# Kernel optimization log

Hardware: AMD Instinct MI355X
Metric: run time of the kernel (lower is better)

## Reference

```python
import jax, jax.numpy as jnp
import numpy as np
from jax import lax

T, B = 128, 256          # rollout length x num envs
H, W, C = 7, 7, 3        # minigrid obs
HID = 128                # lstm hidden
NA = 7                   # actions
NFLAT = 64 * 4 * 4       # conv flatten (7->6->5->4)


def setup_inputs() -> dict:
    key = jax.random.key(0)
    ks = jax.random.split(key, 20)
    N = T * B
    obs = jax.random.randint(ks[0], (N, H, W, C), 0, 11).astype(jnp.float32)
    done = (jax.random.uniform(ks[1], (N,)) < 0.05).astype(jnp.float32)
    h0 = jnp.zeros((1, B, HID), jnp.float32)
    c0 = jnp.zeros((1, B, HID), jnp.float32)
    s = 0.1
    conv1_w = jax.random.normal(ks[2], (16, C, 2, 2)) * s
    conv1_b = jnp.zeros((16,), jnp.float32)
    conv2_w = jax.random.normal(ks[3], (32, 16, 2, 2)) * s
    conv2_b = jnp.zeros((32,), jnp.float32)
    conv3_w = jax.random.normal(ks[4], (64, 32, 2, 2)) * s
    conv3_b = jnp.zeros((64,), jnp.float32)
    w_ih = jax.random.normal(ks[5], (4 * HID, NFLAT)) * 0.03
    w_hh = jax.random.normal(ks[6], (4 * HID, HID)) * 0.08
    b_ih = jnp.zeros((4 * HID,), jnp.float32)
    b_hh = jnp.zeros((4 * HID,), jnp.float32)
    actor_w = jax.random.normal(ks[7], (NA, HID)) * 0.01
    actor_b = jnp.zeros((NA,), jnp.float32)
    critic_w = jax.random.normal(ks[8], (1, HID)) * 0.08
    critic_b = jnp.zeros((1,), jnp.float32)
    return dict(obs=obs, done=done, h0=h0, c0=c0,
                conv1_w=conv1_w, conv1_b=conv1_b,
                conv2_w=conv2_w, conv2_b=conv2_b,
                conv3_w=conv3_w, conv3_b=conv3_b,
                w_ih=w_ih, w_hh=w_hh, b_ih=b_ih, b_hh=b_hh,
                actor_w=actor_w, actor_b=actor_b,
                critic_w=critic_w, critic_b=critic_b)


def _conv(x, w, b):
    # x: [N, Cin, h, w], w: [Cout, Cin, 2, 2], VALID, stride 1
    y = lax.conv_general_dilated(x, w, (1, 1), 'VALID',
                                 dimension_numbers=('NCHW', 'OIHW', 'NCHW'))
    return jax.nn.relu(y + b[None, :, None, None])


def reference(obs, done, h0, c0,
              conv1_w, conv1_b, conv2_w, conv2_b, conv3_w, conv3_b,
              w_ih, w_hh, b_ih, b_hh, actor_w, actor_b, critic_w, critic_b):
    N = obs.shape[0]
    x = jnp.transpose(obs, (0, 3, 1, 2))            # NHWC -> NCHW
    x = _conv(x, conv1_w, conv1_b)
    x = _conv(x, conv2_w, conv2_b)
    x = _conv(x, conv3_w, conv3_b)
    feat = x.reshape(N, -1)                          # [T*B, 1024]

    nb = h0.shape[1]
    xs = feat.reshape(-1, nb, feat.shape[-1])        # [T, B, 1024]
    ds = done.reshape(-1, nb)                        # [T, B]
    bias = b_ih + b_hh

    def step(carry, inp):
        h, c = carry                                  # [B, HID]
        x_t, d_t = inp
        m = (1.0 - d_t)[:, None]
        h = m * h
        c = m * c
        gates = x_t @ w_ih.T + h @ w_hh.T + bias      # [B, 4*HID]
        i, f, g, o = jnp.split(gates, 4, axis=-1)     # torch gate order i,f,g,o
        i = jax.nn.sigmoid(i)
        f = jax.nn.sigmoid(f)
        g = jnp.tanh(g)
        o = jax.nn.sigmoid(o)
        c = f * c + i * g
        h = o * jnp.tanh(c)
        return (h, c), h

    (hT, cT), hs = lax.scan(step, (h0[0], c0[0]), (xs, ds))
    hid = hs.reshape(N, -1)                           # [T*B, HID]
    logits = hid @ actor_w.T + actor_b                # [T*B, NA]
    value = hid @ critic_w.T + critic_b               # [T*B, 1]
    out = jnp.concatenate([logits, value], axis=-1)   # [T*B, NA+1]
    return out, hT[None], cT[None]
```

## Files before the change

### kernel.cpp

```cpp
#include <hip/hip_runtime.h>
#include <hip/hip_bf16.h>


#define N_IMG   32768
#define T_LEN   128
#define B_ENV   256
#define HID     128

typedef _Float16 f16x8 __attribute__((ext_vector_type(8)));
typedef _Float16 f16x2 __attribute__((ext_vector_type(2)));
typedef float    f32x4 __attribute__((ext_vector_type(4)));
typedef unsigned short ushort8v __attribute__((ext_vector_type(8)));
typedef unsigned short ushort4v __attribute__((ext_vector_type(4)));

__device__ __forceinline__ float sigm_(float x) { return 1.0f / (1.0f + __expf(-x)); }
__device__ __forceinline__ float tanh_(float x) { return 2.0f / (1.0f + __expf(-2.0f * x)) - 1.0f; }

__device__ __forceinline__ unsigned short f2h(float x) {
    _Float16 h = (_Float16)x;
    union { _Float16 h; unsigned short u; } un; un.h = h;
    return un.u;
}

#if defined(__has_builtin)
#if __has_builtin(__builtin_amdgcn_fdot2)
#define HAVE_FDOT2 1
#endif
#endif

__device__ __forceinline__ float dot2_(f16x2 a, f16x2 b, float c) {
#ifdef HAVE_FDOT2
    return __builtin_amdgcn_fdot2(a, b, c, false);
#else
    c = fmaf((float)a[0], (float)b[0], c);
    return fmaf((float)a[1], (float)b[1], c);
#endif
}

#define P0(v) __builtin_shufflevector(v, v, 0, 1)
#define P1(v) __builtin_shufflevector(v, v, 2, 3)
#define P2(v) __builtin_shufflevector(v, v, 4, 5)
#define P3(v) __builtin_shufflevector(v, v, 6, 7)

__device__ __forceinline__ float bfly_sum4(float x) {
    int y = __builtin_amdgcn_update_dpp(0, __float_as_int(x), 0xB1, 0xF, 0xF, true);
    x += __int_as_float(y);
    y = __builtin_amdgcn_update_dpp(0, __float_as_int(x), 0x4E, 0xF, 0xF, true);
    return x + __int_as_float(y);
}

#define GLDS16(g, l) __builtin_amdgcn_global_load_lds( \
    (const __attribute__((address_space(1))) unsigned int*)(g), \
    (__attribute__((address_space(3))) unsigned int*)(l), 16, 0, 0)

__global__ void prep_wih(const float* __restrict__ w, unsigned short* __restrict__ wb)
{
    const int idx = blockIdx.x * 256 + threadIdx.x;
    const int np = idx >> 10, kk = idx & 1023;
    const int p = kk >> 6, co = kk & 63;
    const int g = np & 3, ci = np >> 2;
    const int n = g * 128 + ci;
    wb[idx] = f2h(w[n * 1024 + co * 16 + p]);
}

__global__ void prep_convw(const float* __restrict__ w2, const float* __restrict__ w3,
                           unsigned short* __restrict__ wb2g, unsigned short* __restrict__ wb3g)
{
    const int t = blockIdx.x * 256 + threadIdx.x;
    if (t < 2048) {
        const int j = t & 7, lane = (t >> 3) & 63, f = t >> 9;
        const int ky = f >> 1, ct = f & 1;
        const int k = ((lane >> 4) << 3) + j, kx = k >> 4, ci = k & 15;
        wb2g[t] = f2h(w2[(ct * 16 + (lane & 15)) * 64 + ci * 4 + ky * 2 + kx]);
    } else if (t < 10240) {
        const int u = t - 2048;
        const int j = u & 7, lane = (u >> 3) & 63, f = u >> 9;
        const int ct = f >> 2, pos = f & 3;
        const int ci = ((lane >> 4) << 3) + j;
        wb3g[u] = f2h(w3[(ct * 16 + (lane & 15)) * 128 + ci * 4 + pos]);
    }
}

__global__ void prep_whhr(const float* __restrict__ w_hh, unsigned short* __restrict__ whhr)
{
    const int idx = blockIdx.x * 256 + threadIdx.x;
    const int thr = idx >> 7, r = idx & 127;
    const int g = r >> 5, k = r & 31;
    const int ci = thr >> 2, s = thr & 3;
    whhr[idx] = f2h(w_hh[(g * 128 + ci) * 128 + s * 32 + k]);
}

__global__ __launch_bounds__(256, 2) void conv_fused(
    const float* __restrict__ obs,
    const float* __restrict__ w1, const float* __restrict__ b1,
    const float* __restrict__ b2, const float* __restrict__ b3,
    const unsigned short* __restrict__ wb2g,
    const unsigned short* __restrict__ wb3g,
    unsigned short* __restrict__ featb)
{
    __shared__ __align__(16) unsigned char u1[25856];
    __shared__ __align__(16) unsigned char u2[33024];
    __shared__ float w1s[192];
    __shared__ float b1s[16];

    float* s_obs = (float*)u1;
    unsigned short* c2s = (unsigned short*)u1;
    unsigned short* c1s = (unsigned short*)u2;
    unsigned short* c3s = (unsigned short*)u2;

    const int tid = threadIdx.x, lane = tid & 63, wv = tid >> 6;
    const int base = blockIdx.x * 16;

    if (tid < 192) w1s[tid] = w1[tid];
    if (tid < 16)  b1s[tid] = b1[tid];
    for (int i = tid; i < 16 * 147; i += 256) {
        const int im = i / 147, r = i - im * 147;
        s_obs[im * 148 + r] = obs[(size_t)(base + im) * 147 + r];
    }
    __syncthreads();

    {
        const int img = tid & 15;
        const float* ob = &s_obs[img * 148];
        for (int p = tid >> 4; p < 36; p += 16) {
            const int py = p / 6, px = p % 6;
            float o[12];
#pragma unroll
            for (int ky = 0; ky < 2; ky++)
#pragma unroll
                for (int kx = 0; kx < 2; kx++)
#pragma unroll
                    for (int cc = 0; cc < 3; cc++)
                        o[cc * 4 + ky * 2 + kx] = ob[((py + ky) * 7 + px + kx) * 3 + cc];
            unsigned short res[16];
#pragma unroll
            for (int ci = 0; ci < 16; ci++) {
                float a = b1s[ci];
#pragma unroll
                for (int q = 0; q < 12; q++) a = fmaf(o[q], w1s[ci * 12 + q], a);
                res[ci] = f2h(fmaxf(a, 0.0f));
            }
            *(ushort8v*)&c1s[img * 584 + p * 16]     = *(ushort8v*)&res[0];
            *(ushort8v*)&c1s[img * 584 + p * 16 + 8] = *(ushort8v*)&res[8];
        }
    }
    __syncthreads();

    {
        const int ct = wv & 1, par = wv >> 1;
        const int img = lane & 15, kq = lane >> 4;
        f16x8 wA[2];
        wA[0] = *(const f16x8*)&wb2g[(0 + ct) * 512 + lane * 8];
        wA[1] = *(const f16x8*)&wb2g[(2 + ct) * 512 + lane * 8];
        const float4 b2v = *(const float4*)&b2[ct * 16 + kq * 4];
#pragma unroll 2
        for (int p = par; p < 25; p += 2) {
            const int py = p / 5, px = p % 5;
            f32x4 acc = {0.f, 0.f, 0.f, 0.f};
#pragma unroll
            for (int ky = 0; ky < 2; ky++) {
                const int pix = (py + ky) * 6 + px + (kq >> 1);
                const f16x8 bv = *(const f16x8*)&c1s[img * 584 + pix * 16 + (kq & 1) * 8];
                acc = __builtin_amdgcn_mfma_f32_16x16x32_f16(wA[ky], bv, acc, 0, 0, 0);
            }
            unsigned short r4[4];
            r4[0] = f2h(fmaxf(acc[0] + b2v.x, 0.0f));
            r4[1] = f2h(fmaxf(acc[1] + b2v.y, 0.0f));
            r4[2] = f2h(fmaxf(acc[2] + b2v.z, 0.0f));
            r4[3] = f2h(fmaxf(acc[3] + b2v.w, 0.0f));
            *(ushort4v*)&c2s[img * 808 + p * 32 + ct * 16 + kq * 4] = *(ushort4v*)&r4[0];
        }
    }
    __syncthreads();

    {
        const int ct = wv;
        const int img = lane & 15, kq = lane >> 4;
        f16x8 wA3[4];
#pragma unroll
        for (int pos = 0; pos < 4; pos++)
            wA3[pos] = *(const f16x8*)&wb3g[(ct * 4 + pos) * 512 + lane * 8];
        const float4 b3v = *(const float4*)&b3[ct * 16 + kq * 4];
#pragma unroll 4
        for (int p = 0; p < 16; p++) {
            const int py = p >> 2, px = p & 3;
            f32x4 acc = {0.f, 0.f, 0.f, 0.f};
#pragma unroll
            for (int pos = 0; pos < 4; pos++) {
                const int pix = (py + (pos >> 1)) * 5 + px + (pos & 1);
                const f16x8 bv = *(const f16x8*)&c2s[img * 808 + pix * 32 + kq * 8];
                acc = __builtin_amdgcn_mfma_f32_16x16x32_f16(wA3[pos], bv, acc, 0, 0, 0);
            }
            unsigned short r4[4];
            r4[0] = f2h(fmaxf(acc[0] + b3v.x, 0.0f));
            r4[1] = f2h(fmaxf(acc[1] + b3v.y, 0.0f));
            r4[2] = f2h(fmaxf(acc[2] + b3v.z, 0.0f));
            r4[3] = f2h(fmaxf(acc[3] + b3v.w, 0.0f));
            *(ushort4v*)&c3s[img * 1032 + p * 64 + ct * 16 + kq * 4] = *(ushort4v*)&r4[0];
        }
    }
    __syncthreads();

#pragma unroll
    for (int i = 0; i < 8; i++) {
        const int gi = i * 2048 + tid * 8;
        const int img = gi >> 10, flat = gi & 1023;
        *(ushort8v*)&featb[(size_t)(base + img) * 1024 + flat] =
            *(const ushort8v*)&c3s[img * 1032 + flat];
    }
}

__global__ __launch_bounds__(256, 2) void gemm_xproj_mfma(
    const unsigned short* __restrict__ A,
    const unsigned short* __restrict__ W,
    float* __restrict__ C)
{
    __shared__ unsigned short As[128 * 32];
    __shared__ unsigned short Bs[128 * 32];

    const int tid  = threadIdx.x;
    const int bx = blockIdx.x & 3;
    const int by = blockIdx.x >> 2;
    const int m0 = by * 128, n0 = bx * 128;
    const int lane = tid & 63, wave = tid >> 6;
    const int wm = (wave >> 1) * 64, wn = (wave & 1) * 64;
    const int srow = tid >> 2, sseg = tid & 3;

    const unsigned short* Ag = A + (size_t)(m0 + srow) * 1024 + sseg * 8;
    const unsigned short* Wg = W + (size_t)(n0 + srow) * 1024 + sseg * 8;

    f32x4 acc[4][4];
#pragma unroll
    for (int i = 0; i < 4; i++)
#pragma unroll
        for (int j = 0; j < 4; j++) acc[i][j] = (f32x4){0.f, 0.f, 0.f, 0.f};

    const int fr = lane & 15, fq = lane >> 4;

    for (int k0 = 0; k0 < 1024; k0 += 32) {
        __syncthreads();
        GLDS16(Ag + k0,             (char*)As + tid * 16);
        GLDS16(Ag + k0 + 64 * 1024, (char*)As + tid * 16 + 4096);
        GLDS16(Wg + k0,             (char*)Bs + tid * 16);
        GLDS16(Wg + k0 + 64 * 1024, (char*)Bs + tid * 16 + 4096);
        __syncthreads();

        f16x8 af[4], bfv[4];
#pragma unroll
        for (int i = 0; i < 4; i++)
            af[i] = *(const f16x8*)&As[(wm + i * 16 + fr) * 32 + fq * 8];
#pragma unroll
        for (int j = 0; j < 4; j++)
            bfv[j] = *(const f16x8*)&Bs[(wn + j * 16 + fr) * 32 + fq * 8];
#pragma unroll
        for (int i = 0; i < 4; i++)
#pragma unroll
            for (int j = 0; j < 4; j++)
                acc[i][j] = __builtin_amdgcn_mfma_f32_16x16x32_f16(af[i], bfv[j], acc[i][j], 0, 0, 0);
    }

    const int cr = fq * 4, cc = fr;
#pragma unroll
    for (int i = 0; i < 4; i++) {
#pragma unroll
        for (int j = 0; j < 4; j++) {
            float* cp = &C[(size_t)(m0 + wm + i * 16 + cr) * 512 + (n0 + wn + j * 16 + cc)];
#pragma unroll
            for (int r = 0; r < 4; r++)
                cp[(size_t)r * 512] = acc[i][j][r];
        }
    }
}

__global__ __launch_bounds__(512) __attribute__((amdgpu_waves_per_eu(2, 2)))
void lstm_bfly(
    const float* __restrict__ xproj, const float* __restrict__ done,
    const float* __restrict__ h0, const float* __restrict__ c0,
    const unsigned short* __restrict__ whhr,
    const float* __restrict__ b_ih, const float* __restrict__ b_hh,
    float* __restrict__ hid, float* __restrict__ out)
{
    const int b   = blockIdx.x;
    const int tid = threadIdx.x;
    const int ci  = tid >> 2;
    const int s   = tid & 3;

    __shared__ __align__(16) _Float16 hbuf[2][HID];

    f16x8 w[4][4];
    {
        const unsigned short* wp = whhr + (size_t)tid * 128;
#pragma unroll
        for (int g = 0; g < 4; g++)
#pragma unroll
            for (int i = 0; i < 4; i++)
                w[g][i] = *(const f16x8*)&wp[g * 32 + i * 8];
    }
    const float bias_l = b_ih[s * 128 + ci] + b_hh[s * 128 + ci];

    float c = c0[b * HID + ci];
    float h = h0[b * HID + ci];
    float dcur = done[b];

    if (tid < HID)
        hbuf[0][tid] = (_Float16)(h0[b * HID + tid] * (1.0f - dcur));

    float xq = bias_l + xproj[(size_t)b * 512 + ci * 4 + s];
    __syncthreads();

#define DOTBLK(i, c0_, c1_, c2_, c3_)                                           \
    {                                                                           \
        const f16x8 hv8 = *(const f16x8*)&hbuf[p][s * 32 + (i) * 8];            \
        const f16x2 hp0 = P0(hv8), hp1 = P1(hv8), hp2 = P2(hv8), hp3 = P3(hv8); \
        c0_ = dot2_(P0(w[0][i]), hp0, c0_); c0_ = dot2_(P1(w[0][i]), hp1, c0_); \
        c0_ = dot2_(P2(w[0][i]), hp2, c0_); c0_ = dot2_(P3(w[0][i]), hp3, c0_); \
        c1_ = dot2_(P0(w[1][i]), hp0, c1_); c1_ = dot2_(P1(w[1][i]), hp1, c1_); \
        c1_ = dot2_(P2(w[1][i]), hp2, c1_); c1_ = dot2_(P3(w[1][i]), hp3, c1_); \
        c2_ = dot2_(P0(w[2][i]), hp0, c2_); c2_ = dot2_(P1(w[2][i]), hp1, c2_); \
        c2_ = dot2_(P2(w[2][i]), hp2, c2_); c2_ = dot2_(P3(w[2][i]), hp3, c2_); \
        c3_ = dot2_(P0(w[3][i]), hp0, c3_); c3_ = dot2_(P1(w[3][i]), hp1, c3_); \
        c3_ = dot2_(P2(w[3][i]), hp2, c3_); c3_ = dot2_(P3(w[3][i]), hp3, c3_); \
    }

    int p = 0;
    for (int t = 0; t < T_LEN; t++) {
        const int tn = (t + 1 < T_LEN) ? t + 1 : t;
        const float xqn = bias_l + xproj[((size_t)tn * B_ENV + b) * 512 + ci * 4 + s];
        const float dnn = done[tn * B_ENV + b];

        float a0 = (s == 0) ? xq : 0.0f;
        float a1 = (s == 1) ? xq : 0.0f;
        float a2 = (s == 2) ? xq : 0.0f;
        float a3 = (s == 3) ? xq : 0.0f;
        float b0 = 0.f, b1 = 0.f, b2 = 0.f, b3 = 0.f;
        DOTBLK(0, a0, a1, a2, a3)
        DOTBLK(1, b0, b1, b2, b3)
        DOTBLK(2, a0, a1, a2, a3)
        DOTBLK(3, b0, b1, b2, b3)
        a0 += b0; a1 += b1; a2 += b2; a3 += b3;

        a0 = bfly_sum4(a0); a1 = bfly_sum4(a1);
        a2 = bfly_sum4(a2); a3 = bfly_sum4(a3);

        const float gi = sigm_(a0), gf = sigm_(a1);
        const float gg = tanh_(a2), go = sigm_(a3);
        const float m = 1.0f - dcur;
        c = fmaf(gf, c * m, gi * gg);
        h = go * tanh_(c);

        if (s == 0) {
            hid[((size_t)t * B_ENV + b) * HID + ci] = h;
            hbuf[p ^ 1][ci] = (_Float16)(h * (1.0f - dnn));
        }

        xq = xqn; dcur = dnn; p ^= 1;
        __syncthreads();
    }

    if (s == 0) {
        out[262144 + b * HID + ci] = h;
        out[294912 + b * HID + ci] = c;
    }
#undef DOTBLK
}

__global__ __launch_bounds__(256, 2) void heads_kernel(
    const float* __restrict__ hid,
    const float* __restrict__ aw, const float* __restrict__ ab,
    const float* __restrict__ cw, const float* __restrict__ cb,
    float* __restrict__ out)
{
    __shared__ float hs[32 * 129];
    __shared__ float ws[8 * 130];
    __shared__ float bs[8];

    const int tid = threadIdx.x;
    const int n0 = blockIdx.x * 32;

    for (int i = tid; i < 1024; i += 256) {
        const int r = i >> 7, k = i & 127;
        ws[r * 130 + k] = (r < 7) ? aw[r * 128 + k] : cw[k];
    }
    if (tid < 8) bs[tid] = (tid < 7) ? ab[tid] : cb[0];
    for (int i = tid; i < 4096; i += 256) {
        const int r = i >> 7, k = i & 127;
        hs[r * 129 + k] = hid[(size_t)(n0 + r) * 128 + k];
    }
    __syncthreads();

    const int r = tid >> 3, jj = tid & 7;
    float acc = bs[jj];
    const float* hp = &hs[r * 129];
    const float* wp = &ws[jj * 130];
#pragma unroll
    for (int k = 0; k < 128; k++) acc = fmaf(hp[k], wp[k], acc);
    out[(size_t)(n0 + r) * 8 + jj] = acc;
}

extern "C" void kernel_launch(void* const* d_in, const int* in_sizes, int n_in,
                              void* d_out, int out_size, void* d_ws, size_t ws_size,
                              hipStream_t stream)
{
    (void)in_sizes; (void)n_in; (void)out_size; (void)ws_size;

    const float* obs  = (const float*)d_in[0];
    const float* done = (const float*)d_in[1];
    const float* h0   = (const float*)d_in[2];
    const float* c0   = (const float*)d_in[3];
    const float* w1   = (const float*)d_in[4];
    const float* b1   = (const float*)d_in[5];
    const float* w2   = (const float*)d_in[6];
    const float* b2   = (const float*)d_in[7];
    const float* w3   = (const float*)d_in[8];
    const float* b3   = (const float*)d_in[9];
    const float* w_ih = (const float*)d_in[10];
    const float* w_hh = (const float*)d_in[11];
    const float* b_ih = (const float*)d_in[12];
    const float* b_hh = (const float*)d_in[13];
    const float* aw   = (const float*)d_in[14];
    const float* ab   = (const float*)d_in[15];
    const float* cw   = (const float*)d_in[16];
    const float* cb   = (const float*)d_in[17];
    float* out = (float*)d_out;

    unsigned short* featb = (unsigned short*)d_ws;
    unsigned short* wb    = featb + 33554432ull;
    unsigned short* wb2g  = wb    + 524288ull;
    unsigned short* wb3g  = wb2g  + 2048ull;
    float* xproj = (float*)(wb3g + 8192ull + 2048ull);
    float* hid   = xproj + 16777216ull;
    unsigned short* whhr = (unsigned short*)(hid + 4194304ull);

    prep_wih<<<2048, 256, 0, stream>>>(w_ih, wb);
    prep_convw<<<40, 256, 0, stream>>>(w2, w3, wb2g, wb3g);
    prep_whhr<<<256, 256, 0, stream>>>(w_hh, whhr);
    conv_fused<<<2048, 256, 0, stream>>>(obs, w1, b1, b2, b3, wb2g, wb3g, featb);
    gemm_xproj_mfma<<<1024, 256, 0, stream>>>(featb, wb, xproj);
    lstm_bfly<<<256, 512, 0, stream>>>(xproj, done, h0, c0, whhr, b_ih, b_hh, hid, out);
    heads_kernel<<<1024, 256, 0, stream>>>(hid, aw, ab, cw, cb, out);
}
```

Baseline: 309.5 us.

## Double-buffer xproj GEMM, fuse prep kernels, fp16 hidden states, faster activations

Several independent changes. The sigmoid and tanh helpers now use the exp2 and reciprocal hardware builtins. The three weight-prep kernels are merged into one launch. The input-projection GEMM double-buffers its LDS tiles so the next K-slice loads while MFMAs run. The LSTM hidden-state history is stored as fp16 and widened back to fp32 in the heads kernel, halving that traffic at some precision cost. The LSTM's serial recurrence probably dominates total time, so the gains elsewhere may be small.

After: 281.6 us. -9.0%, faster.

```diff
diff --git a/kernel.cpp b/kernel.cpp
--- a/kernel.cpp
+++ b/kernel.cpp
@@ -13,8 +13,27 @@
 typedef unsigned short ushort8v __attribute__((ext_vector_type(8)));
 typedef unsigned short ushort4v __attribute__((ext_vector_type(4)));
 
-__device__ __forceinline__ float sigm_(float x) { return 1.0f / (1.0f + __expf(-x)); }
-__device__ __forceinline__ float tanh_(float x) { return 2.0f / (1.0f + __expf(-2.0f * x)) - 1.0f; }
+#if defined(__has_builtin)
+#if __has_builtin(__builtin_amdgcn_exp2f)
+#define FEXP2(x) __builtin_amdgcn_exp2f(x)
+#endif
+#if __has_builtin(__builtin_amdgcn_rcpf)
+#define FRCP(x) __builtin_amdgcn_rcpf(x)
+#endif
+#endif
+#ifndef FEXP2
+#define FEXP2(x) exp2f(x)
+#endif
+#ifndef FRCP
+#define FRCP(x) (1.0f / (x))
+#endif
+
+__device__ __forceinline__ float sigm_(float x) {
+    return FRCP(1.0f + FEXP2(-1.44269504f * x));
+}
+__device__ __forceinline__ float tanh_(float x) {
+    return fmaf(-2.0f, FRCP(1.0f + FEXP2(2.88539008f * x)), 1.0f);
+}
 
 __device__ __forceinline__ unsigned short f2h(float x) {
     _Float16 h = (_Float16)x;
@@ -53,41 +72,39 @@
     (const __attribute__((address_space(1))) unsigned int*)(g), \
     (__attribute__((address_space(3))) unsigned int*)(l), 16, 0, 0)
 
-__global__ void prep_wih(const float* __restrict__ w, unsigned short* __restrict__ wb)
-{
-    const int idx = blockIdx.x * 256 + threadIdx.x;
-    const int np = idx >> 10, kk = idx & 1023;
-    const int p = kk >> 6, co = kk & 63;
-    const int g = np & 3, ci = np >> 2;
-    const int n = g * 128 + ci;
-    wb[idx] = f2h(w[n * 1024 + co * 16 + p]);
-}
-
-__global__ void prep_convw(const float* __restrict__ w2, const float* __restrict__ w3,
-                           unsigned short* __restrict__ wb2g, unsigned short* __restrict__ wb3g)
-{
-    const int t = blockIdx.x * 256 + threadIdx.x;
-    if (t < 2048) {
-        const int j = t & 7, lane = (t >> 3) & 63, f = t >> 9;
-        const int ky = f >> 1, ct = f & 1;
-        const int k = ((lane >> 4) << 3) + j, kx = k >> 4, ci = k & 15;
-        wb2g[t] = f2h(w2[(ct * 16 + (lane & 15)) * 64 + ci * 4 + ky * 2 + kx]);
-    } else if (t < 10240) {
-        const int u = t - 2048;
-        const int j = u & 7, lane = (u >> 3) & 63, f = u >> 9;
-        const int ct = f >> 2, pos = f & 3;
-        const int ci = ((lane >> 4) << 3) + j;
-        wb3g[u] = f2h(w3[(ct * 16 + (lane & 15)) * 128 + ci * 4 + pos]);
-    }
-}
-
-__global__ void prep_whhr(const float* __restrict__ w_hh, unsigned short* __restrict__ whhr)
-{
-    const int idx = blockIdx.x * 256 + threadIdx.x;
-    const int thr = idx >> 7, r = idx & 127;
-    const int g = r >> 5, k = r & 31;
-    const int ci = thr >> 2, s = thr & 3;
-    whhr[idx] = f2h(w_hh[(g * 128 + ci) * 128 + s * 32 + k]);
+__global__ void prep_all(const float* __restrict__ w_ih, unsigned short* __restrict__ wb,
+                         const float* __restrict__ w2, const float* __restrict__ w3,
+                         unsigned short* __restrict__ wb2g, unsigned short* __restrict__ wb3g,
+                         const float* __restrict__ w_hh, unsigned short* __restrict__ whhr)
+{
+    const int bid = blockIdx.x, tid = threadIdx.x;
+    if (bid < 2048) {
+        const int idx = bid * 256 + tid;
+        const int np = idx >> 10, kk = idx & 1023;
+        const int p = kk >> 6, co = kk & 63;
+        const int g = np & 3, ci = np >> 2;
+        wb[idx] = f2h(w_ih[(g * 128 + ci) * 1024 + co * 16 + p]);
+    } else if (bid < 2088) {
+        const int t = (bid - 2048) * 256 + tid;
+        if (t < 2048) {
+            const int j = t & 7, lane = (t >> 3) & 63, f = t >> 9;
+            const int ky = f >> 1, ct = f & 1;
+            const int k = ((lane >> 4) << 3) + j, kx = k >> 4, ci = k & 15;
+            wb2g[t] = f2h(w2[(ct * 16 + (lane & 15)) * 64 + ci * 4 + ky * 2 + kx]);
+        } else {
+            const int u = t - 2048;
+            const int j = u & 7, lane = (u >> 3) & 63, f = u >> 9;
+            const int ct = f >> 2, pos = f & 3;
+            const int ci = ((lane >> 4) << 3) + j;
+            wb3g[u] = f2h(w3[(ct * 16 + (lane & 15)) * 128 + ci * 4 + pos]);
+        }
+    } else {
+        const int idx = (bid - 2088) * 256 + tid;
+        const int thr = idx >> 7, r = idx & 127;
+        const int g = r >> 5, k = r & 31;
+        const int ci = thr >> 2, s = thr & 3;
+        whhr[idx] = f2h(w_hh[(g * 128 + ci) * 128 + s * 32 + k]);
+    }
 }
 
 __global__ __launch_bounds__(256, 2) void conv_fused(
@@ -215,8 +232,8 @@
     const unsigned short* __restrict__ W,
     float* __restrict__ C)
 {
-    __shared__ unsigned short As[128 * 32];
-    __shared__ unsigned short Bs[128 * 32];
+    __shared__ unsigned short As[2][128 * 32];
+    __shared__ unsigned short Bs[2][128 * 32];
 
     const int tid  = threadIdx.x;
     const int bx = blockIdx.x & 3;
@@ -237,27 +254,39 @@
 
     const int fr = lane & 15, fq = lane >> 4;
 
-    for (int k0 = 0; k0 < 1024; k0 += 32) {
-        __syncthreads();
-        GLDS16(Ag + k0,             (char*)As + tid * 16);
-        GLDS16(Ag + k0 + 64 * 1024, (char*)As + tid * 16 + 4096);
-        GLDS16(Wg + k0,             (char*)Bs + tid * 16);
-        GLDS16(Wg + k0 + 64 * 1024, (char*)Bs + tid * 16 + 4096);
-        __syncthreads();
+#define STAGEK(bb, k0) do {                                                \
+        GLDS16(Ag + (k0),             (char*)&As[bb][0] + tid * 16);       \
+        GLDS16(Ag + (k0) + 64 * 1024, (char*)&As[bb][0] + tid * 16 + 4096);\
+        GLDS16(Wg + (k0),             (char*)&Bs[bb][0] + tid * 16);       \
+        GLDS16(Wg + (k0) + 64 * 1024, (char*)&Bs[bb][0] + tid * 16 + 4096);\
+    } while (0)
+
+    STAGEK(0, 0);
+    asm volatile("s_waitcnt vmcnt(0)" ::: "memory");
+    __syncthreads();
+
+    int cur = 0;
+    for (int ks = 0; ks < 32; ks++) {
+        if (ks + 1 < 32) STAGEK(cur ^ 1, (ks + 1) * 32);
 
         f16x8 af[4], bfv[4];
 #pragma unroll
         for (int i = 0; i < 4; i++)
-            af[i] = *(const f16x8*)&As[(wm + i * 16 + fr) * 32 + fq * 8];
+            af[i] = *(const f16x8*)&As[cur][(wm + i * 16 + fr) * 32 + fq * 8];
 #pragma unroll
         for (int j = 0; j < 4; j++)
-            bfv[j] = *(const f16x8*)&Bs[(wn + j * 16 + fr) * 32 + fq * 8];
+            bfv[j] = *(const f16x8*)&Bs[cur][(wn + j * 16 + fr) * 32 + fq * 8];
 #pragma unroll
         for (int i = 0; i < 4; i++)
 #pragma unroll
             for (int j = 0; j < 4; j++)
                 acc[i][j] = __builtin_amdgcn_mfma_f32_16x16x32_f16(af[i], bfv[j], acc[i][j], 0, 0, 0);
-    }
+
+        asm volatile("s_waitcnt vmcnt(0)" ::: "memory");
+        __syncthreads();
+        cur ^= 1;
+    }
+#undef STAGEK
 
     const int cr = fq * 4, cc = fr;
 #pragma unroll
@@ -278,7 +307,7 @@
     const float* __restrict__ h0, const float* __restrict__ c0,
     const unsigned short* __restrict__ whhr,
     const float* __restrict__ b_ih, const float* __restrict__ b_hh,
-    float* __restrict__ hid, float* __restrict__ out)
+    unsigned short* __restrict__ hid16, float* __restrict__ out)
 {
     const int b   = blockIdx.x;
     const int tid = threadIdx.x;
@@ -349,7 +378,7 @@
         h = go * tanh_(c);
 
         if (s == 0) {
-            hid[((size_t)t * B_ENV + b) * HID + ci] = h;
+            hid16[((size_t)t * B_ENV + b) * HID + ci] = f2h(h);
             hbuf[p ^ 1][ci] = (_Float16)(h * (1.0f - dnn));
         }
 
@@ -365,7 +394,7 @@
 }
 
 __global__ __launch_bounds__(256, 2) void heads_kernel(
-    const float* __restrict__ hid,
+    const unsigned short* __restrict__ hid16,
     const float* __restrict__ aw, const float* __restrict__ ab,
     const float* __restrict__ cw, const float* __restrict__ cb,
     float* __restrict__ out)
@@ -382,9 +411,14 @@
         ws[r * 130 + k] = (r < 7) ? aw[r * 128 + k] : cw[k];
     }
     if (tid < 8) bs[tid] = (tid < 7) ? ab[tid] : cb[0];
-    for (int i = tid; i < 4096; i += 256) {
-        const int r = i >> 7, k = i & 127;
-        hs[r * 129 + k] = hid[(size_t)(n0 + r) * 128 + k];
+    for (int i = tid; i < 512; i += 256) {
+        const int r = i >> 4, k8 = (i & 15) * 8;
+        const ushort8v v = *(const ushort8v*)&hid16[(size_t)(n0 + r) * 128 + k8];
+#pragma unroll
+        for (int q = 0; q < 8; q++) {
+            union { unsigned short u; _Float16 h; } un; un.u = v[q];
+            hs[r * 129 + k8 + q] = (float)un.h;
+        }
     }
     __syncthreads();
 
@@ -428,14 +462,12 @@
     unsigned short* wb2g  = wb    + 524288ull;
     unsigned short* wb3g  = wb2g  + 2048ull;
     float* xproj = (float*)(wb3g + 8192ull + 2048ull);
-    float* hid   = xproj + 16777216ull;
-    unsigned short* whhr = (unsigned short*)(hid + 4194304ull);
-
-    prep_wih<<<2048, 256, 0, stream>>>(w_ih, wb);
-    prep_convw<<<40, 256, 0, stream>>>(w2, w3, wb2g, wb3g);
-    prep_whhr<<<256, 256, 0, stream>>>(w_hh, whhr);
+    unsigned short* hid16 = (unsigned short*)(xproj + 16777216ull);
+    unsigned short* whhr  = hid16 + 4194304ull;
+
+    prep_all<<<2344, 256, 0, stream>>>(w_ih, wb, w2, w3, wb2g, wb3g, w_hh, whhr);
     conv_fused<<<2048, 256, 0, stream>>>(obs, w1, b1, b2, b3, wb2g, wb3g, featb);
     gemm_xproj_mfma<<<1024, 256, 0, stream>>>(featb, wb, xproj);
-    lstm_bfly<<<256, 512, 0, stream>>>(xproj, done, h0, c0, whhr, b_ih, b_hh, hid, out);
-    heads_kernel<<<1024, 256, 0, stream>>>(hid, aw, ab, cw, cb, out);
-}
+    lstm_bfly<<<256, 512, 0, stream>>>(xproj, done, h0, c0, whhr, b_ih, b_hh, hid16, out);
+    heads_kernel<<<1024, 256, 0, stream>>>(hid16, aw, ab, cw, cb, out);
+}
```
